# Performance work log

Measured on AMD Instinct MI355X. Metric: run time of the kernel, lower is better.

The kernel has to match this reference:

```python
import jax, jax.numpy as jnp
import numpy as np

N = 8192
QS = 128
KS = 128
F = 256
EPS = 1e-5     # BatchNorm1d default eps
SLOPE = 0.01   # LeakyReLU default negative_slope


def _leaky(x):
    return jnp.where(x >= 0, x, SLOPE * x)


def _mlp_bn(x, w1, b1, w2, b2, gamma, beta):
    # Sequential(Linear, LeakyReLU, Linear, LeakyReLU) then BatchNorm1d (training mode)
    h = _leaky(x @ w1 + b1)
    h = _leaky(h @ w2 + b2)
    mean = h.mean(axis=0)
    var = h.var(axis=0)  # biased variance, as torch BN uses for normalization
    return gamma * (h - mean) * jax.lax.rsqrt(var + EPS) + beta


def setup_inputs() -> dict:
    key = jax.random.key(0)
    ks = jax.random.split(key, 24)

    def lin_w(k_, fi, fo):
        s = 1.0 / np.sqrt(fi)
        return jax.random.uniform(k_, (fi, fo), minval=-s, maxval=s, dtype=jnp.float32)

    def lin_b(k_, fi, fo):
        s = 1.0 / np.sqrt(fi)
        return jax.random.uniform(k_, (fo,), minval=-s, maxval=s, dtype=jnp.float32)

    A = (jax.random.uniform(ks[0], (N, N)) < 0.004).astype(jnp.float32)
    q = jax.random.normal(ks[1], (N, QS), dtype=jnp.float32)
    k = jax.random.normal(ks[2], (N, KS), dtype=jnp.float32)

    inp = {"A": A, "q": q, "k": k}
    i = 3
    for pre, fi in (("q", QS), ("k", KS), ("v", KS)):
        inp[pre + "_w1"] = lin_w(ks[i], fi, F); i += 1
        inp[pre + "_b1"] = lin_b(ks[i], fi, F); i += 1
        inp[pre + "_w2"] = lin_w(ks[i], F, F); i += 1
        inp[pre + "_b2"] = lin_b(ks[i], F, F); i += 1
        inp[pre + "_gamma"] = jnp.ones((F,), jnp.float32)
        inp[pre + "_beta"] = jnp.zeros((F,), jnp.float32)
    return inp


def reference(A, q, k,
              q_w1, q_b1, q_w2, q_b2, q_gamma, q_beta,
              k_w1, k_b1, k_w2, k_b2, k_gamma, k_beta,
              v_w1, v_b1, v_w2, v_b2, v_gamma, v_beta):
    qe1 = _mlp_bn(q, q_w1, q_b1, q_w2, q_b2, q_gamma, q_beta)   # [N, F]
    ke1 = _mlp_bn(k, k_w1, k_b1, k_w2, k_b2, k_gamma, k_beta)   # [N, F]
    prod = (qe1 @ ke1.T) / jnp.sqrt(jnp.float32(F))             # [N, N]
    # NOTE: faithful to source — mask zeroes scores (not -inf) before softmax
    masked = A * prod
    attn = jax.nn.softmax(masked, axis=1)
    ve1 = _mlp_bn(k, v_w1, v_b1, v_w2, v_b2, v_gamma, v_beta)   # [N, F]
    return attn @ ve1                                            # [N, F]
```

## Files before the change

kernel.cpp:

```cpp
#include <hip/hip_runtime.h>

#define NROWS 8192
#define FDIM 256
#define CAP 128

typedef _Float16 half8_t __attribute__((ext_vector_type(8)));
typedef _Float16 half4_t __attribute__((ext_vector_type(4)));
typedef float floatx4 __attribute__((ext_vector_type(4)));

struct MlpPtrs {
  const float* w1[3]; const float* b1[3];
  const float* w2[3]; const float* b2[3];
  const float* gamma[3]; const float* beta[3];
};

__global__ __launch_bounds__(256) void prep_kernel(
    const float* __restrict__ q, const float* __restrict__ k, MlpPtrs p,
    _Float16* __restrict__ qh, _Float16* __restrict__ kh,
    _Float16* __restrict__ w1p, _Float16* __restrict__ w2p) {
  int task = blockIdx.y;
  int tid = blockIdx.x * 256 + threadIdx.x;
  if (task == 0) { if (tid < NROWS * 128) qh[tid] = (_Float16)q[tid]; return; }
  if (task == 1) { if (tid < NROWS * 128) kh[tid] = (_Float16)k[tid]; return; }
  int m = (task - 2) % 3;
  bool isw2 = task >= 5;
  int K = isw2 ? 256 : 128;
  if (tid >= K * 256) return;
  const float* src = isw2 ? p.w2[m] : p.w1[m];
  _Float16* dst = isw2 ? (w2p + m * 65536) : (w1p + m * 32768);
  int j = tid & 7, lane = (tid >> 3) & 63, rest = tid >> 9;
  int ktiles = K >> 5;
  int k_tile = rest % ktiles, n_tile = rest / ktiles;
  int kk = k_tile * 32 + (lane >> 4) * 8 + j;
  int nn = n_tile * 16 + (lane & 15);
  dst[tid] = (_Float16)src[kk * 256 + nn];
}

__global__ __launch_bounds__(256) void gemm1_kernel(
    const _Float16* __restrict__ qh, const _Float16* __restrict__ kh,
    const _Float16* __restrict__ w1p, MlpPtrs p, _Float16* __restrict__ h1) {
  const int mlp = blockIdx.z;
  const _Float16* X = (mlp == 0) ? qh : kh;
  const _Float16* wp = w1p + mlp * 32768;
  _Float16* out = h1 + (size_t)mlp * (NROWS * FDIM);
  const float* bias = p.b1[mlp];
  int lane = threadIdx.x & 63, wave = threadIdx.x >> 6;
  int lm = lane & 15, lq = lane >> 4;
  int m0 = blockIdx.x * 64 + wave * 16;
  int n0 = blockIdx.y * 64;
  floatx4 acc[4];
  #pragma unroll
  for (int t = 0; t < 4; ++t) acc[t] = (floatx4){0.f, 0.f, 0.f, 0.f};
  const half8_t* ap = (const half8_t*)(X + (size_t)(m0 + lm) * 128 + lq * 8);
  const half8_t* wp8 = (const half8_t*)wp;
  #pragma unroll
  for (int kt = 0; kt < 4; ++kt) {
    half8_t a = ap[kt * 4];
    #pragma unroll
    for (int t = 0; t < 4; ++t) {
      half8_t b = wp8[(((n0 >> 4) + t) * 4 + kt) * 64 + lane];
      acc[t] = __builtin_amdgcn_mfma_f32_16x16x32_f16(a, b, acc[t], 0, 0, 0);
    }
  }
  #pragma unroll
  for (int t = 0; t < 4; ++t) {
    int col = n0 + t * 16 + lm;
    float bb = bias[col];
    #pragma unroll
    for (int r = 0; r < 4; ++r) {
      float v = acc[t][r] + bb;
      v = (v >= 0.f) ? v : 0.01f * v;
      out[(size_t)(m0 + lq * 4 + r) * FDIM + col] = (_Float16)v;
    }
  }
}

__global__ __launch_bounds__(256) void gemm2_kernel(
    const _Float16* __restrict__ h1, const _Float16* __restrict__ w2p,
    MlpPtrs p, _Float16* __restrict__ e1,
    float* __restrict__ colsum, float* __restrict__ colsumsq) {
  const int mlp = blockIdx.z;
  const _Float16* X = h1 + (size_t)mlp * (NROWS * FDIM);
  const _Float16* wp = w2p + mlp * 65536;
  _Float16* out = e1 + (size_t)mlp * (NROWS * FDIM);
  const float* bias = p.b2[mlp];
  int lane = threadIdx.x & 63, wave = threadIdx.x >> 6;
  int lm = lane & 15, lq = lane >> 4;
  int m0 = blockIdx.x * 64 + wave * 16;
  int n0 = blockIdx.y * 64;
  floatx4 acc[4];
  #pragma unroll
  for (int t = 0; t < 4; ++t) acc[t] = (floatx4){0.f, 0.f, 0.f, 0.f};
  const half8_t* ap = (const half8_t*)(X + (size_t)(m0 + lm) * 256 + lq * 8);
  const half8_t* wp8 = (const half8_t*)wp;
  #pragma unroll
  for (int kt = 0; kt < 8; ++kt) {
    half8_t a = ap[kt * 4];
    #pragma unroll
    for (int t = 0; t < 4; ++t) {
      half8_t b = wp8[(((n0 >> 4) + t) * 8 + kt) * 64 + lane];
      acc[t] = __builtin_amdgcn_mfma_f32_16x16x32_f16(a, b, acc[t], 0, 0, 0);
    }
  }
  #pragma unroll
  for (int t = 0; t < 4; ++t) {
    int col = n0 + t * 16 + lm;
    float bb = bias[col];
    float s = 0.f, s2 = 0.f;
    #pragma unroll
    for (int r = 0; r < 4; ++r) {
      float v = acc[t][r] + bb;
      v = (v >= 0.f) ? v : 0.01f * v;
      out[(size_t)(m0 + lq * 4 + r) * FDIM + col] = (_Float16)v;
      s += v; s2 += v * v;
    }
    s  += __shfl_xor(s, 16, 64);  s  += __shfl_xor(s, 32, 64);
    s2 += __shfl_xor(s2, 16, 64); s2 += __shfl_xor(s2, 32, 64);
    if (lq == 0) {
      atomicAdd(&colsum[mlp * FDIM + col], s);
      atomicAdd(&colsumsq[mlp * FDIM + col], s2);
    }
  }
}

__global__ __launch_bounds__(256) void norm_kernel(
    _Float16* __restrict__ e1, const float* __restrict__ colsum,
    const float* __restrict__ colsumsq, MlpPtrs p, float* __restrict__ S_all) {
  int mlp = blockIdx.y;
  int c = threadIdx.x;
  _Float16* h = e1 + (size_t)mlp * (NROWS * FDIM);
  float mean = colsum[mlp * FDIM + c] * (1.f / NROWS);
  float var = colsumsq[mlp * FDIM + c] * (1.f / NROWS) - mean * mean;
  float scale = p.gamma[mlp][c] * rsqrtf(var + 1e-5f);
  float shift = p.beta[mlp][c] - mean * scale;
  int r0 = blockIdx.x * 32;
  float sv = 0.f;
  for (int r = 0; r < 32; ++r) {
    size_t idx = (size_t)(r0 + r) * FDIM + c;
    float v = (float)h[idx] * scale + shift;
    _Float16 hv = (_Float16)v;
    h[idx] = hv;
    sv += (float)hv;
  }
  if (mlp == 2) atomicAdd(&S_all[c], sv);
}

__global__ __launch_bounds__(256) void attn_kernel(
    const float* __restrict__ A,
    const _Float16* __restrict__ e1, const float* __restrict__ S_all,
    float* __restrict__ out) {
  const _Float16* qe = e1;
  const _Float16* ke = e1 + (size_t)1 * NROWS * FDIM;
  const _Float16* ve = e1 + (size_t)2 * NROWS * FDIM;
  int i = blockIdx.x;
  int tid = threadIdx.x, lane = tid & 63, wave = tid >> 6;
  __shared__ int sj[CAP];
  __shared__ float sw[CAP];
  __shared__ float pacc[4][FDIM];
  __shared__ int s_cnt;
  __shared__ float sm_em, sm_inv;
  if (tid == 0) s_cnt = 0;
  __syncthreads();

  const floatx4* row = (const floatx4*)(A + (size_t)i * NROWS);
  #pragma unroll
  for (int it = 0; it < 8; ++it) {
    int v4 = it * 256 + tid;
    floatx4 v = __builtin_nontemporal_load(&row[v4]);
    int cols[4]; int c = 0;
    if (v[0] != 0.f) cols[c++] = v4 * 4 + 0;
    if (v[1] != 0.f) cols[c++] = v4 * 4 + 1;
    if (v[2] != 0.f) cols[c++] = v4 * 4 + 2;
    if (v[3] != 0.f) cols[c++] = v4 * 4 + 3;
    if (c) {
      int pos = atomicAdd(&s_cnt, c);
      for (int l = 0; l < c; ++l) if (pos + l < CAP) sj[pos + l] = cols[l];
    }
  }
  __syncthreads();
  int nnz = s_cnt < CAP ? s_cnt : CAP;

  half4_t qv = *(const half4_t*)(qe + (size_t)i * FDIM + 4 * lane);
  float q0 = qv[0], q1 = qv[1], q2 = qv[2], q3 = qv[3];
  for (int e = wave; e < nnz; e += 4) {
    int j = sj[e];
    half4_t kv = *(const half4_t*)(ke + (size_t)j * FDIM + 4 * lane);
    float s = q0 * (float)kv[0] + q1 * (float)kv[1] + q2 * (float)kv[2] + q3 * (float)kv[3];
    #pragma unroll
    for (int off = 32; off >= 1; off >>= 1) s += __shfl_xor(s, off, 64);
    if (lane == 0) sw[e] = s * 0.0625f;
  }
  __syncthreads();

  if (wave == 0) {
    bool v0ok = lane < nnz, v1ok = lane + 64 < nnz;
    float v0 = v0ok ? sw[lane] : 0.f;
    float v1 = v1ok ? sw[lane + 64] : 0.f;
    float lm = fmaxf(fmaxf(v0, v1), 0.f);
    #pragma unroll
    for (int off = 32; off >= 1; off >>= 1) lm = fmaxf(lm, __shfl_xor(lm, off, 64));
    float m = lm;
    float em = expf(-m);
    float w0 = v0ok ? expf(v0 - m) : 0.f;
    float w1 = v1ok ? expf(v1 - m) : 0.f;
    float ls = w0 + w1;
    #pragma unroll
    for (int off = 32; off >= 1; off >>= 1) ls += __shfl_xor(ls, off, 64);
    if (v0ok) sw[lane] = w0 - em;
    if (v1ok) sw[lane + 64] = w1 - em;
    if (lane == 0) {
      sm_em = em;
      sm_inv = 1.f / (ls + (float)(NROWS - nnz) * em);
    }
  }
  __syncthreads();

  float a0 = 0.f, a1 = 0.f, a2 = 0.f, a3 = 0.f;
  for (int e = wave; e < nnz; e += 4) {
    int j = sj[e];
    float w = sw[e];
    half4_t vv = *(const half4_t*)(ve + (size_t)j * FDIM + 4 * lane);
    a0 += w * (float)vv[0];
    a1 += w * (float)vv[1];
    a2 += w * (float)vv[2];
    a3 += w * (float)vv[3];
  }
  ((floatx4*)pacc[wave])[lane] = (floatx4){a0, a1, a2, a3};
  __syncthreads();

  int c = tid;
  float em = sm_em, inv = sm_inv;
  float s = pacc[0][c] + pacc[1][c] + pacc[2][c] + pacc[3][c] + em * S_all[c];
  __builtin_nontemporal_store(s * inv, &out[(size_t)i * FDIM + c]);
}

extern "C" void kernel_launch(void* const* d_in, const int* in_sizes, int n_in,
                              void* d_out, int out_size, void* d_ws, size_t ws_size,
                              hipStream_t stream) {
  const float* A = (const float*)d_in[0];
  const float* q = (const float*)d_in[1];
  const float* k = (const float*)d_in[2];
  MlpPtrs p;
  for (int m = 0; m < 3; ++m) {
    const int b = 3 + m * 6;
    p.w1[m]    = (const float*)d_in[b + 0];
    p.b1[m]    = (const float*)d_in[b + 1];
    p.w2[m]    = (const float*)d_in[b + 2];
    p.b2[m]    = (const float*)d_in[b + 3];
    p.gamma[m] = (const float*)d_in[b + 4];
    p.beta[m]  = (const float*)d_in[b + 5];
  }
  char* ws = (char*)d_ws;
  const size_t MB = 1024 * 1024;
  _Float16* qh  = (_Float16*)(ws + 0);
  _Float16* kh  = (_Float16*)(ws + 2 * MB);
  _Float16* h1  = (_Float16*)(ws + 4 * MB);
  _Float16* e1  = (_Float16*)(ws + 16 * MB);
  _Float16* w1p = (_Float16*)(ws + 28 * MB);
  _Float16* w2p = (_Float16*)(ws + 28 * MB + 192 * 1024);
  float* colsum   = (float*)(ws + 28 * MB + 640 * 1024);
  float* colsumsq = colsum + 3 * FDIM;
  float* S_all    = colsumsq + 3 * FDIM;

  (void)hipMemsetAsync(colsum, 0, 7 * 1024, stream);
  prep_kernel<<<dim3(4096, 8, 1), 256, 0, stream>>>(q, k, p, qh, kh, w1p, w2p);
  gemm1_kernel<<<dim3(128, 4, 3), 256, 0, stream>>>(qh, kh, w1p, p, h1);
  gemm2_kernel<<<dim3(128, 4, 3), 256, 0, stream>>>(h1, w2p, p, e1, colsum, colsumsq);
  norm_kernel<<<dim3(256, 3, 1), 256, 0, stream>>>(e1, colsum, colsumsq, p, S_all);
  attn_kernel<<<NROWS, 256, 0, stream>>>(A, e1, S_all, (float*)d_out);
}
```

Measured before the change: 488.0 us.

## Batch adjacency loads, split edges across lane groups, fold softmax into waves

The attention kernel now issues all eight adjacency-row loads before scanning them, so more memory requests are in flight per thread. The score dot products use 16-lane groups with half8 loads, so each wave handles four edges at once with a shorter shuffle reduction. Every wave now computes the softmax max and sum itself, removing a barrier and the shared scalars, and the exponentials are recomputed inside the V accumulation, which uses half8 loads with two edges per wave. The prep kernel converts q and k with vectorised grid-stride loops on a much smaller grid; the cost is repeated exp work in each wave and higher register pressure from the preloaded row.

```diff
diff --git a/kernel.cpp b/kernel.cpp
--- a/kernel.cpp
+++ b/kernel.cpp
@@ -20,8 +20,17 @@
     _Float16* __restrict__ w1p, _Float16* __restrict__ w2p) {
   int task = blockIdx.y;
   int tid = blockIdx.x * 256 + threadIdx.x;
-  if (task == 0) { if (tid < NROWS * 128) qh[tid] = (_Float16)q[tid]; return; }
-  if (task == 1) { if (tid < NROWS * 128) kh[tid] = (_Float16)k[tid]; return; }
+  if (task < 2) {
+    const float* src = task == 0 ? q : k;
+    _Float16* dst = task == 0 ? qh : kh;
+    const floatx4* s4 = (const floatx4*)src;
+    half4_t* d4 = (half4_t*)dst;
+    for (int idx = tid; idx < (NROWS * 128) / 4; idx += 256 * 256) {
+      floatx4 v = s4[idx];
+      d4[idx] = (half4_t){(_Float16)v[0], (_Float16)v[1], (_Float16)v[2], (_Float16)v[3]};
+    }
+    return;
+  }
   int m = (task - 2) % 3;
   bool isw2 = task >= 5;
   int K = isw2 ? 256 : 128;
@@ -158,20 +167,22 @@
   __shared__ float sw[CAP];
   __shared__ float pacc[4][FDIM];
   __shared__ int s_cnt;
-  __shared__ float sm_em, sm_inv;
   if (tid == 0) s_cnt = 0;
   __syncthreads();
 
   const floatx4* row = (const floatx4*)(A + (size_t)i * NROWS);
+  floatx4 av[8];
+  #pragma unroll
+  for (int it = 0; it < 8; ++it)
+    av[it] = __builtin_nontemporal_load(&row[it * 256 + tid]);
   #pragma unroll
   for (int it = 0; it < 8; ++it) {
     int v4 = it * 256 + tid;
-    floatx4 v = __builtin_nontemporal_load(&row[v4]);
     int cols[4]; int c = 0;
-    if (v[0] != 0.f) cols[c++] = v4 * 4 + 0;
-    if (v[1] != 0.f) cols[c++] = v4 * 4 + 1;
-    if (v[2] != 0.f) cols[c++] = v4 * 4 + 2;
-    if (v[3] != 0.f) cols[c++] = v4 * 4 + 3;
+    if (av[it][0] != 0.f) cols[c++] = v4 * 4 + 0;
+    if (av[it][1] != 0.f) cols[c++] = v4 * 4 + 1;
+    if (av[it][2] != 0.f) cols[c++] = v4 * 4 + 2;
+    if (av[it][3] != 0.f) cols[c++] = v4 * 4 + 3;
     if (c) {
       int pos = atomicAdd(&s_cnt, c);
       for (int l = 0; l < c; ++l) if (pos + l < CAP) sj[pos + l] = cols[l];
@@ -180,56 +191,60 @@
   __syncthreads();
   int nnz = s_cnt < CAP ? s_cnt : CAP;
 
-  half4_t qv = *(const half4_t*)(qe + (size_t)i * FDIM + 4 * lane);
-  float q0 = qv[0], q1 = qv[1], q2 = qv[2], q3 = qv[3];
-  for (int e = wave; e < nnz; e += 4) {
+  int cl = lane & 15, g = lane >> 4;
+  const half8_t* qe8 = (const half8_t*)(qe + (size_t)i * FDIM + cl * 16);
+  half8_t qa = qe8[0], qb = qe8[1];
+  for (int e = wave * 4 + g; e < nnz; e += 16) {
     int j = sj[e];
-    half4_t kv = *(const half4_t*)(ke + (size_t)j * FDIM + 4 * lane);
-    float s = q0 * (float)kv[0] + q1 * (float)kv[1] + q2 * (float)kv[2] + q3 * (float)kv[3];
-    #pragma unroll
-    for (int off = 32; off >= 1; off >>= 1) s += __shfl_xor(s, off, 64);
-    if (lane == 0) sw[e] = s * 0.0625f;
-  }
-  __syncthreads();
-
-  if (wave == 0) {
-    bool v0ok = lane < nnz, v1ok = lane + 64 < nnz;
-    float v0 = v0ok ? sw[lane] : 0.f;
-    float v1 = v1ok ? sw[lane + 64] : 0.f;
-    float lm = fmaxf(fmaxf(v0, v1), 0.f);
-    #pragma unroll
-    for (int off = 32; off >= 1; off >>= 1) lm = fmaxf(lm, __shfl_xor(lm, off, 64));
-    float m = lm;
-    float em = expf(-m);
-    float w0 = v0ok ? expf(v0 - m) : 0.f;
-    float w1 = v1ok ? expf(v1 - m) : 0.f;
-    float ls = w0 + w1;
-    #pragma unroll
-    for (int off = 32; off >= 1; off >>= 1) ls += __shfl_xor(ls, off, 64);
-    if (v0ok) sw[lane] = w0 - em;
-    if (v1ok) sw[lane + 64] = w1 - em;
-    if (lane == 0) {
-      sm_em = em;
-      sm_inv = 1.f / (ls + (float)(NROWS - nnz) * em);
-    }
-  }
-  __syncthreads();
-
-  float a0 = 0.f, a1 = 0.f, a2 = 0.f, a3 = 0.f;
-  for (int e = wave; e < nnz; e += 4) {
+    const half8_t* ke8 = (const half8_t*)(ke + (size_t)j * FDIM + cl * 16);
+    half8_t ka = ke8[0], kb = ke8[1];
+    float s = 0.f;
+    #pragma unroll
+    for (int r = 0; r < 8; ++r)
+      s += (float)qa[r] * (float)ka[r] + (float)qb[r] * (float)kb[r];
+    #pragma unroll
+    for (int off = 8; off >= 1; off >>= 1) s += __shfl_xor(s, off, 64);
+    if (cl == 0) sw[e] = s * 0.0625f;
+  }
+  __syncthreads();
+
+  float v0 = lane < nnz ? sw[lane] : 0.f;
+  float v1 = lane + 64 < nnz ? sw[lane + 64] : 0.f;
+  float m = fmaxf(fmaxf(v0, v1), 0.f);
+  #pragma unroll
+  for (int off = 32; off >= 1; off >>= 1) m = fmaxf(m, __shfl_xor(m, off, 64));
+  float em = __expf(-m);
+  float w0 = lane < nnz ? __expf(v0 - m) : 0.f;
+  float w1 = lane + 64 < nnz ? __expf(v1 - m) : 0.f;
+  float ls = w0 + w1;
+  #pragma unroll
+  for (int off = 32; off >= 1; off >>= 1) ls += __shfl_xor(ls, off, 64);
+  float inv = 1.f / (ls + (float)(NROWS - nnz) * em);
+
+  int par = lane >> 5, c8 = lane & 31;
+  floatx4 accA = (floatx4){0.f, 0.f, 0.f, 0.f};
+  floatx4 accB = (floatx4){0.f, 0.f, 0.f, 0.f};
+  for (int e = wave * 2 + par; e < nnz; e += 8) {
     int j = sj[e];
-    float w = sw[e];
-    half4_t vv = *(const half4_t*)(ve + (size_t)j * FDIM + 4 * lane);
-    a0 += w * (float)vv[0];
-    a1 += w * (float)vv[1];
-    a2 += w * (float)vv[2];
-    a3 += w * (float)vv[3];
-  }
-  ((floatx4*)pacc[wave])[lane] = (floatx4){a0, a1, a2, a3};
+    float w = __expf(sw[e] - m) - em;
+    half8_t vv = *(const half8_t*)(ve + (size_t)j * FDIM + c8 * 8);
+    accA[0] += w * (float)vv[0]; accA[1] += w * (float)vv[1];
+    accA[2] += w * (float)vv[2]; accA[3] += w * (float)vv[3];
+    accB[0] += w * (float)vv[4]; accB[1] += w * (float)vv[5];
+    accB[2] += w * (float)vv[6]; accB[3] += w * (float)vv[7];
+  }
+  #pragma unroll
+  for (int r = 0; r < 4; ++r) {
+    accA[r] += __shfl_xor(accA[r], 32, 64);
+    accB[r] += __shfl_xor(accB[r], 32, 64);
+  }
+  if (par == 0) {
+    ((floatx4*)&pacc[wave][c8 * 8])[0] = accA;
+    ((floatx4*)&pacc[wave][c8 * 8])[1] = accB;
+  }
   __syncthreads();
 
   int c = tid;
-  float em = sm_em, inv = sm_inv;
   float s = pacc[0][c] + pacc[1][c] + pacc[2][c] + pacc[3][c] + em * S_all[c];
   __builtin_nontemporal_store(s * inv, &out[(size_t)i * FDIM + c]);
 }
@@ -263,7 +278,7 @@
   float* S_all    = colsumsq + 3 * FDIM;
 
   (void)hipMemsetAsync(colsum, 0, 7 * 1024, stream);
-  prep_kernel<<<dim3(4096, 8, 1), 256, 0, stream>>>(q, k, p, qh, kh, w1p, w2p);
+  prep_kernel<<<dim3(256, 8, 1), 256, 0, stream>>>(q, k, p, qh, kh, w1p, w2p);
   gemm1_kernel<<<dim3(128, 4, 3), 256, 0, stream>>>(qh, kh, w1p, p, h1);
   gemm2_kernel<<<dim3(128, 4, 3), 256, 0, stream>>>(h1, w2p, p, e1, colsum, colsumsq);
   norm_kernel<<<dim3(256, 3, 1), 256, 0, stream>>>(e1, colsum, colsumsq, p, S_all);
```

Result: faster. 458.0 us (-6.2%).
